# Performance work log

Measured on AMD Instinct MI355X. Metric: run time of the kernel, lower is better.

The kernel has to match this reference:

```python
import jax, jax.numpy as jnp
import numpy as np

# --- module constants (from init_kwargs) ---
BETA = 0.95
UTE = 1.0001
DELAY = 7
CHOSEN_W1 = 0.5
THRESHOLD = 1.0      # snntorch Leaky default threshold
ALPHA = 2.0          # snntorch ATan surrogate default alpha
T, B = 4096, 4096
SPIKE_PROB = 0.02    # sparse binary spike trains


@jax.custom_vjp
def spike_fn(x):
    # Heaviside forward; ATan surrogate gradient in backward (snntorch default)
    return (x > 0).astype(x.dtype)

def _spike_fwd(x):
    return spike_fn(x), x

def _spike_bwd(x, g):
    return (g * (ALPHA / 2.0) / (1.0 + (jnp.pi / 2.0 * ALPHA * x) ** 2),)

spike_fn.defvjp(_spike_fwd, _spike_bwd)


def setup_inputs() -> dict:
    key = jax.random.key(0)
    k1, _ = jax.random.split(key)
    spike_seq = (jax.random.uniform(k1, (T, B, 2)) < SPIKE_PROB).astype(jnp.float32)
    # calculate_weights(delay): w1 = chosen_w1; w2 = ute - beta**delay * w1
    w1 = CHOSEN_W1
    w2 = UTE - BETA ** DELAY * w1
    W = jnp.array([[w1, w2]], dtype=jnp.float32)  # fc.weight, shape [1, 2]
    return {"spike_seq": spike_seq, "W": W}


def reference(spike_seq, W):
    # spike_seq: [T, B, 2], W: [1, 2] -> spk_rec: [T, B, 1]
    # Precompute all linear currents in one GEMM (same math as per-step fc)
    cur_seq = jnp.einsum('tbi,oi->tbo', spike_seq, W)  # [T, B, 1]

    def step(mem, cur):
        # snntorch Leaky (reset_mechanism='subtract'):
        #   reset computed from PREVIOUS mem (detached heaviside)
        reset = (mem > THRESHOLD).astype(mem.dtype)
        mem_new = BETA * mem + cur - reset * THRESHOLD
        spk = spike_fn(mem_new - THRESHOLD)
        return mem_new, spk

    mem0 = jnp.zeros((spike_seq.shape[1], 1), dtype=spike_seq.dtype)
    _, spk_rec = jax.lax.scan(step, mem0, cur_seq)
    return spk_rec
```

## Files before the change

kernel.cpp:

```cpp
#include <hip/hip_runtime.h>
#include <stdint.h>


#define T_STEPS 4096
#define B_NEUR  4096
#define NCHUNK  32
#define CH_W    8
#define WARM_W  48
#define KG      (T_STEPS / 16)
#define NWORDS  (T_STEPS / 32)

typedef float f4v __attribute__((ext_vector_type(4)));

__global__ __launch_bounds__(256) void fmfm_compress(
    const f4v*  __restrict__ sp4,
    uint32_t*   __restrict__ codes)
{
    const int tid = blockIdx.x * 256 + threadIdx.x;
    const int b2  = tid & (B_NEUR / 2 - 1);
    const int kg  = tid >> 11;
    const f4v* p = sp4 + (size_t)kg * 16 * (B_NEUR / 2) + b2;
    uint32_t we = 0, wo = 0;
    #pragma unroll
    for (int i = 0; i < 16; ++i) {
        f4v s = __builtin_nontemporal_load(p + (size_t)i * (B_NEUR / 2));
        uint32_t ce = (s.x != 0.0f ? 1u : 0u) | (s.y != 0.0f ? 2u : 0u);
        uint32_t co = (s.z != 0.0f ? 1u : 0u) | (s.w != 0.0f ? 2u : 0u);
        we |= ce << (2 * i);
        wo |= co << (2 * i);
    }
    *reinterpret_cast<uint2*>(codes + (size_t)kg * B_NEUR + 2 * b2) =
        make_uint2(we, wo);
}

__global__ __launch_bounds__(256, 2) void fmfm_scanA(
    const uint32_t* __restrict__ codes,
    const float*    __restrict__ W,
    uint32_t*       __restrict__ bits_out,
    uint4*          __restrict__ spec)
{
    __shared__ float2 lut2[16];

    const float w1  = W[0];
    const float w2  = W[1];
    const float w12 = __fadd_rn(w1, w2);

    if (threadIdx.x < 16) {
        uint32_t e = threadIdx.x;
        uint32_t c0 = e & 3u, c1 = (e >> 2) & 3u;
        float2 v;
        v.x = (c0 & 1u) ? ((c0 & 2u) ? w12 : w1) : ((c0 & 2u) ? w2 : 0.0f);
        v.y = (c1 & 1u) ? ((c1 & 2u) ? w12 : w1) : ((c1 & 2u) ? w2 : 0.0f);
        lut2[e] = v;
    }
    __syncthreads();

    const int tid = blockIdx.x * 256 + threadIdx.x;
    const int b   = tid & (B_NEUR - 1);
    const int c   = tid >> 12;
    const int body_w0 = c * CH_W;
    const int w_start = (body_w0 >= WARM_W) ? body_w0 - WARM_W : 0;
    const int w_end   = body_w0 + CH_W;
    const uint32_t* cp = codes + b;

#define CLD(IDX) cp[(size_t)((IDX) < w_end ? (IDX) : (w_end - 1)) * B_NEUR]
#define DECODE2(WORD, D)                                                  \
    {                                                                     \
        _Pragma("unroll")                                                 \
        for (int _j = 0; _j < 8; ++_j)                                    \
            D[_j] = lut2[((WORD) >> (4 * _j)) & 0xFu];                    \
    }
#define STEPN(CUR)                                                        \
    {                                                                     \
        float _m = __fsub_rn(__fadd_rn(__fmul_rn(0.95f, mem), (CUR)),     \
                             rst);                                        \
        rst = (_m > 1.0f) ? 1.0f : 0.0f;                                  \
        mem = _m;                                                         \
    }
#define STEPB(CUR, POS)                                                   \
    {                                                                     \
        float _m = __fsub_rn(__fadd_rn(__fmul_rn(0.95f, mem), (CUR)),     \
                             rst);                                        \
        uint32_t _sb = (_m > 1.0f) ? 1u : 0u;                             \
        bits |= _sb << (POS);                                             \
        rst = _sb ? 1.0f : 0.0f;                                          \
        mem = _m;                                                         \
    }
#define CHAIN16N(D)                                                       \
    {                                                                     \
        _Pragma("unroll")                                                 \
        for (int _j = 0; _j < 8; ++_j) { STEPN(D[_j].x) STEPN(D[_j].y) }  \
    }
#define CHAIN16B(D, HALF)                                                 \
    {                                                                     \
        _Pragma("unroll")                                                 \
        for (int _j = 0; _j < 8; ++_j) {                                  \
            STEPB(D[_j].x, ((HALF) << 4) + 2 * _j)                        \
            STEPB(D[_j].y, ((HALF) << 4) + 2 * _j + 1)                    \
        }                                                                 \
    }
#define PF8(G)                                                            \
    t0 = CLD((G) + 8);  t1 = CLD((G) + 9);  t2 = CLD((G) + 10);           \
    t3 = CLD((G) + 11); t4 = CLD((G) + 12); t5 = CLD((G) + 13);           \
    t6 = CLD((G) + 14); t7 = CLD((G) + 15);
#define ROT8()                                                            \
    c0 = t0; c1 = t1; c2 = t2; c3 = t3;                                   \
    c4 = t4; c5 = t5; c6 = t6; c7 = t7;
#define STB(IDX) bits_out[(size_t)(IDX) * B_NEUR + b] = bits;

    uint32_t c0 = CLD(w_start);     uint32_t c1 = CLD(w_start + 1);
    uint32_t c2 = CLD(w_start + 2); uint32_t c3 = CLD(w_start + 3);
    uint32_t c4 = CLD(w_start + 4); uint32_t c5 = CLD(w_start + 5);
    uint32_t c6 = CLD(w_start + 6); uint32_t c7 = CLD(w_start + 7);
    uint32_t t0, t1, t2, t3, t4, t5, t6, t7;

    float2 dA[8], dB[8];
    DECODE2(c0, dA)

    float mem = 0.0f, rst = 0.0f;

    for (int g = w_start; g < body_w0; g += 8) {
        PF8(g)
        DECODE2(c1, dB) CHAIN16N(dA)
        DECODE2(c2, dA) CHAIN16N(dB)
        DECODE2(c3, dB) CHAIN16N(dA)
        DECODE2(c4, dA) CHAIN16N(dB)
        DECODE2(c5, dB) CHAIN16N(dA)
        DECODE2(c6, dA) CHAIN16N(dB)
        DECODE2(c7, dB) CHAIN16N(dA)
        DECODE2(t0, dA) CHAIN16N(dB)
        ROT8()
    }

    const float sm = mem;
    const float sr = rst;

    for (int g = body_w0; g < w_end; g += 8) {
        PF8(g)
        uint32_t bits = 0;
        DECODE2(c1, dB) CHAIN16B(dA, 0)
        DECODE2(c2, dA) CHAIN16B(dB, 1) STB((g + 1) >> 1) bits = 0;
        DECODE2(c3, dB) CHAIN16B(dA, 0)
        DECODE2(c4, dA) CHAIN16B(dB, 1) STB((g + 3) >> 1) bits = 0;
        DECODE2(c5, dB) CHAIN16B(dA, 0)
        DECODE2(c6, dA) CHAIN16B(dB, 1) STB((g + 5) >> 1) bits = 0;
        DECODE2(c7, dB) CHAIN16B(dA, 0)
        DECODE2(t0, dA) CHAIN16B(dB, 1) STB((g + 7) >> 1)
        ROT8()
    }

    uint4 sv;
    sv.x = __float_as_uint(sm);
    sv.y = (sr != 0.0f) ? 1u : 0u;
    sv.z = __float_as_uint(mem);
    sv.w = (rst != 0.0f) ? 1u : 0u;
    spec[(size_t)c * B_NEUR + b] = sv;

#undef CLD
#undef DECODE2
#undef STEPN
#undef STEPB
#undef CHAIN16N
#undef CHAIN16B
#undef PF8
#undef ROT8
#undef STB
}

__global__ __launch_bounds__(64) void fmfm_scanB(
    const uint32_t* __restrict__ codes,
    const float*    __restrict__ W,
    uint32_t*       __restrict__ bits_out,
    const uint4*    __restrict__ spec)
{
    const int b = blockIdx.x * 64 + threadIdx.x;
    const float w1  = W[0];
    const float w2  = W[1];
    const float w12 = __fadd_rn(w1, w2);

    float mem = 0.0f, rst = 0.0f;
    uint4 sn = spec[b];
    for (int c = 0; c < NCHUNK; ++c) {
        uint4 s = sn;
        if (c + 1 < NCHUNK) sn = spec[(size_t)(c + 1) * B_NEUR + b];
        bool ok = (s.x == __float_as_uint(mem)) &&
                  ((s.y != 0u) == (rst != 0.0f));
        if (ok) {
            mem = __uint_as_float(s.z);
            rst = s.w ? 1.0f : 0.0f;
        } else {
            uint32_t bits = 0;
            for (int wi = 0; wi < CH_W; ++wi) {
                uint32_t w = codes[(size_t)(c * CH_W + wi) * B_NEUR + b];
                #pragma unroll
                for (int j = 0; j < 16; ++j) {
                    uint32_t cc = (w >> (2 * j)) & 3u;
                    float cur = (cc & 1u) ? ((cc & 2u) ? w12 : w1)
                                          : ((cc & 2u) ? w2 : 0.0f);
                    float m = __fsub_rn(__fadd_rn(__fmul_rn(0.95f, mem), cur),
                                        rst);
                    uint32_t sb = (m > 1.0f) ? 1u : 0u;
                    bits |= sb << (((wi & 1) << 4) + j);
                    rst = sb ? 1.0f : 0.0f;
                    mem = m;
                }
                if (wi & 1) {
                    bits_out[(size_t)((c * CH_W + wi) >> 1) * B_NEUR + b] = bits;
                    bits = 0;
                }
            }
        }
    }
}

__global__ __launch_bounds__(256) void fmfm_expand(
    const uint32_t* __restrict__ bits,
    float*          __restrict__ out)
{
    const int tid = blockIdx.x * 256 + threadIdx.x;
    const int b4  = tid & 1023;
    const int w   = (tid >> 10) & 127;
    const int q   = tid >> 17;
    const uint4 bw = *reinterpret_cast<const uint4*>(
        bits + (size_t)w * B_NEUR + (size_t)b4 * 4);
    float* qp = out + ((size_t)w * 32 + q * 8) * B_NEUR + (size_t)b4 * 4;
    #pragma unroll
    for (int r = 0; r < 8; ++r) {
        const int tp = q * 8 + r;
        f4v v;
        v.x = ((bw.x >> tp) & 1u) ? 1.0f : 0.0f;
        v.y = ((bw.y >> tp) & 1u) ? 1.0f : 0.0f;
        v.z = ((bw.z >> tp) & 1u) ? 1.0f : 0.0f;
        v.w = ((bw.w >> tp) & 1u) ? 1.0f : 0.0f;
        *reinterpret_cast<f4v*>(qp + (size_t)r * B_NEUR) = v;
    }
}

__global__ __launch_bounds__(64) void fmfm_scan_fused(
    const float2* __restrict__ sp, const float* __restrict__ W,
    float* __restrict__ out)
{
    const int b = blockIdx.x * 64 + threadIdx.x;
    const float w1 = W[0];
    const float w2 = W[1];
    const float2* p = sp + b;
    float* q = out + b;
    float mem = 0.0f, rst = 0.0f;
    #pragma unroll 8
    for (int t = 0; t < T_STEPS; ++t) {
        float2 s = p[(size_t)t * B_NEUR];
        float cur = __fadd_rn(__fmul_rn(s.x, w1), __fmul_rn(s.y, w2));
        float m = __fsub_rn(__fadd_rn(__fmul_rn(0.95f, mem), cur), rst);
        float spk = (m > 1.0f) ? 1.0f : 0.0f;
        q[(size_t)t * B_NEUR] = spk;
        mem = m;
        rst = spk;
    }
}

extern "C" void kernel_launch(void* const* d_in, const int* in_sizes, int n_in,
                              void* d_out, int out_size, void* d_ws, size_t ws_size,
                              hipStream_t stream) {
    const f4v*   sp4 = (const f4v*)d_in[0];
    const float* W   = (const float*)d_in[1];
    float*       out = (float*)d_out;

    const size_t codes_bytes = (size_t)KG * B_NEUR * 4;
    const size_t bits_bytes  = (size_t)NWORDS * B_NEUR * 4;
    const size_t spec_bytes  = (size_t)NCHUNK * B_NEUR * 16;
    if (ws_size < codes_bytes + bits_bytes + spec_bytes) {
        fmfm_scan_fused<<<dim3(B_NEUR / 64), dim3(64), 0, stream>>>(
            (const float2*)d_in[0], W, out);
        return;
    }
    uint32_t* codes = (uint32_t*)d_ws;
    uint32_t* bits  = (uint32_t*)((char*)d_ws + codes_bytes);
    uint4*    spec  = (uint4*)((char*)d_ws + codes_bytes + bits_bytes);

    fmfm_compress<<<dim3(KG * (B_NEUR / 2) / 256), dim3(256), 0, stream>>>(sp4, codes);
    fmfm_scanA<<<dim3(NCHUNK * B_NEUR / 256), dim3(256), 0, stream>>>(codes, W, bits, spec);
    fmfm_scanB<<<dim3(B_NEUR / 64), dim3(64), 0, stream>>>(codes, W, bits, spec);
    fmfm_expand<<<dim3(NWORDS * (B_NEUR / 4) * 4 / 256), dim3(256), 0, stream>>>(bits, out);
}
```

Measured before the change: 66.86 us.

## Interleave two independent chunk scans per thread in speculative scan kernel

Each thread of the chunked speculative scan now processes two chunks (c and c+16) at once, interleaving their recurrence steps to expose instruction-level parallelism across two dependent chains. The grid halves to 256 blocks of 256 threads, occupancy hint drops to one block per SIMD group, and the warm-up window handling is restructured with zero-padding for negative indices. This trades thread-level parallelism for ILP and more registers, aiming to hide the serial FP latency of the membrane chain.

```diff
diff --git a/kernel.cpp b/kernel.cpp
--- a/kernel.cpp
+++ b/kernel.cpp
@@ -33,7 +33,7 @@
         make_uint2(we, wo);
 }
 
-__global__ __launch_bounds__(256, 2) void fmfm_scanA(
+__global__ __launch_bounds__(256, 1) void fmfm_scanA2(
     const uint32_t* __restrict__ codes,
     const float*    __restrict__ W,
     uint32_t*       __restrict__ bits_out,
@@ -47,124 +47,148 @@
 
     if (threadIdx.x < 16) {
         uint32_t e = threadIdx.x;
-        uint32_t c0 = e & 3u, c1 = (e >> 2) & 3u;
+        uint32_t q0 = e & 3u, q1 = (e >> 2) & 3u;
         float2 v;
-        v.x = (c0 & 1u) ? ((c0 & 2u) ? w12 : w1) : ((c0 & 2u) ? w2 : 0.0f);
-        v.y = (c1 & 1u) ? ((c1 & 2u) ? w12 : w1) : ((c1 & 2u) ? w2 : 0.0f);
+        v.x = (q0 & 1u) ? ((q0 & 2u) ? w12 : w1) : ((q0 & 2u) ? w2 : 0.0f);
+        v.y = (q1 & 1u) ? ((q1 & 2u) ? w12 : w1) : ((q1 & 2u) ? w2 : 0.0f);
         lut2[e] = v;
     }
     __syncthreads();
 
     const int tid = blockIdx.x * 256 + threadIdx.x;
     const int b   = tid & (B_NEUR - 1);
-    const int c   = tid >> 12;
-    const int body_w0 = c * CH_W;
-    const int w_start = (body_w0 >= WARM_W) ? body_w0 - WARM_W : 0;
-    const int w_end   = body_w0 + CH_W;
-    const uint32_t* cp = codes + b;
-
-#define CLD(IDX) cp[(size_t)((IDX) < w_end ? (IDX) : (w_end - 1)) * B_NEUR]
+    const int cpair = tid >> 12;
+    const int cA  = cpair;
+    const int cB  = cpair + 16;
+    const int wA0 = cA * CH_W - WARM_W;
+    const int wB0 = cB * CH_W - WARM_W;
+    const uint32_t* cptr = codes + b;
+
+#define FA(V) (((wA0 + (V)) < 0) ? 0u                                     \
+                : cptr[(size_t)(wA0 + (V)) * B_NEUR])
+#define FB(V) cptr[(size_t)(wB0 + (V)) * B_NEUR]
 #define DECODE2(WORD, D)                                                  \
     {                                                                     \
         _Pragma("unroll")                                                 \
         for (int _j = 0; _j < 8; ++_j)                                    \
             D[_j] = lut2[((WORD) >> (4 * _j)) & 0xFu];                    \
     }
-#define STEPN(CUR)                                                        \
-    {                                                                     \
-        float _m = __fsub_rn(__fadd_rn(__fmul_rn(0.95f, mem), (CUR)),     \
-                             rst);                                        \
-        rst = (_m > 1.0f) ? 1.0f : 0.0f;                                  \
-        mem = _m;                                                         \
-    }
-#define STEPB(CUR, POS)                                                   \
-    {                                                                     \
-        float _m = __fsub_rn(__fadd_rn(__fmul_rn(0.95f, mem), (CUR)),     \
-                             rst);                                        \
+#define STEPN_A(CUR)                                                      \
+    {                                                                     \
+        float _m = __fsub_rn(__fadd_rn(__fmul_rn(0.95f, memA), (CUR)),    \
+                             rstA);                                       \
+        rstA = (_m > 1.0f) ? 1.0f : 0.0f;                                 \
+        memA = _m;                                                        \
+    }
+#define STEPN_B(CUR)                                                      \
+    {                                                                     \
+        float _m = __fsub_rn(__fadd_rn(__fmul_rn(0.95f, memB), (CUR)),    \
+                             rstB);                                       \
+        rstB = (_m > 1.0f) ? 1.0f : 0.0f;                                 \
+        memB = _m;                                                        \
+    }
+#define STEPB_A(CUR, POS)                                                 \
+    {                                                                     \
+        float _m = __fsub_rn(__fadd_rn(__fmul_rn(0.95f, memA), (CUR)),    \
+                             rstA);                                       \
         uint32_t _sb = (_m > 1.0f) ? 1u : 0u;                             \
-        bits |= _sb << (POS);                                             \
-        rst = _sb ? 1.0f : 0.0f;                                          \
-        mem = _m;                                                         \
-    }
-#define CHAIN16N(D)                                                       \
-    {                                                                     \
-        _Pragma("unroll")                                                 \
-        for (int _j = 0; _j < 8; ++_j) { STEPN(D[_j].x) STEPN(D[_j].y) }  \
-    }
-#define CHAIN16B(D, HALF)                                                 \
+        bitsA |= _sb << (POS);                                            \
+        rstA = _sb ? 1.0f : 0.0f;                                         \
+        memA = _m;                                                        \
+    }
+#define STEPB_B(CUR, POS)                                                 \
+    {                                                                     \
+        float _m = __fsub_rn(__fadd_rn(__fmul_rn(0.95f, memB), (CUR)),    \
+                             rstB);                                       \
+        uint32_t _sb = (_m > 1.0f) ? 1u : 0u;                             \
+        bitsB |= _sb << (POS);                                            \
+        rstB = _sb ? 1.0f : 0.0f;                                         \
+        memB = _m;                                                        \
+    }
+#define CH2N(DA, DB)                                                      \
     {                                                                     \
         _Pragma("unroll")                                                 \
         for (int _j = 0; _j < 8; ++_j) {                                  \
-            STEPB(D[_j].x, ((HALF) << 4) + 2 * _j)                        \
-            STEPB(D[_j].y, ((HALF) << 4) + 2 * _j + 1)                    \
+            STEPN_A(DA[_j].x) STEPN_B(DB[_j].x)                           \
+            STEPN_A(DA[_j].y) STEPN_B(DB[_j].y)                           \
         }                                                                 \
     }
-#define PF8(G)                                                            \
-    t0 = CLD((G) + 8);  t1 = CLD((G) + 9);  t2 = CLD((G) + 10);           \
-    t3 = CLD((G) + 11); t4 = CLD((G) + 12); t5 = CLD((G) + 13);           \
-    t6 = CLD((G) + 14); t7 = CLD((G) + 15);
-#define ROT8()                                                            \
-    c0 = t0; c1 = t1; c2 = t2; c3 = t3;                                   \
-    c4 = t4; c5 = t5; c6 = t6; c7 = t7;
-#define STB(IDX) bits_out[(size_t)(IDX) * B_NEUR + b] = bits;
-
-    uint32_t c0 = CLD(w_start);     uint32_t c1 = CLD(w_start + 1);
-    uint32_t c2 = CLD(w_start + 2); uint32_t c3 = CLD(w_start + 3);
-    uint32_t c4 = CLD(w_start + 4); uint32_t c5 = CLD(w_start + 5);
-    uint32_t c6 = CLD(w_start + 6); uint32_t c7 = CLD(w_start + 7);
-    uint32_t t0, t1, t2, t3, t4, t5, t6, t7;
-
-    float2 dA[8], dB[8];
-    DECODE2(c0, dA)
-
-    float mem = 0.0f, rst = 0.0f;
-
-    for (int g = w_start; g < body_w0; g += 8) {
-        PF8(g)
-        DECODE2(c1, dB) CHAIN16N(dA)
-        DECODE2(c2, dA) CHAIN16N(dB)
-        DECODE2(c3, dB) CHAIN16N(dA)
-        DECODE2(c4, dA) CHAIN16N(dB)
-        DECODE2(c5, dB) CHAIN16N(dA)
-        DECODE2(c6, dA) CHAIN16N(dB)
-        DECODE2(c7, dB) CHAIN16N(dA)
-        DECODE2(t0, dA) CHAIN16N(dB)
-        ROT8()
-    }
-
-    const float sm = mem;
-    const float sr = rst;
-
-    for (int g = body_w0; g < w_end; g += 8) {
-        PF8(g)
-        uint32_t bits = 0;
-        DECODE2(c1, dB) CHAIN16B(dA, 0)
-        DECODE2(c2, dA) CHAIN16B(dB, 1) STB((g + 1) >> 1) bits = 0;
-        DECODE2(c3, dB) CHAIN16B(dA, 0)
-        DECODE2(c4, dA) CHAIN16B(dB, 1) STB((g + 3) >> 1) bits = 0;
-        DECODE2(c5, dB) CHAIN16B(dA, 0)
-        DECODE2(c6, dA) CHAIN16B(dB, 1) STB((g + 5) >> 1) bits = 0;
-        DECODE2(c7, dB) CHAIN16B(dA, 0)
-        DECODE2(t0, dA) CHAIN16B(dB, 1) STB((g + 7) >> 1)
-        ROT8()
-    }
-
-    uint4 sv;
-    sv.x = __float_as_uint(sm);
-    sv.y = (sr != 0.0f) ? 1u : 0u;
-    sv.z = __float_as_uint(mem);
-    sv.w = (rst != 0.0f) ? 1u : 0u;
-    spec[(size_t)c * B_NEUR + b] = sv;
-
-#undef CLD
+#define CH2B(DA, DB, HALF)                                                \
+    {                                                                     \
+        _Pragma("unroll")                                                 \
+        for (int _j = 0; _j < 8; ++_j) {                                  \
+            STEPB_A(DA[_j].x, ((HALF) << 4) + 2 * _j)                     \
+            STEPB_B(DB[_j].x, ((HALF) << 4) + 2 * _j)                     \
+            STEPB_A(DA[_j].y, ((HALF) << 4) + 2 * _j + 1)                 \
+            STEPB_B(DB[_j].y, ((HALF) << 4) + 2 * _j + 1)                 \
+        }                                                                 \
+    }
+
+    uint32_t a1 = FA(1), a2 = FA(2), a3 = FA(3), a4 = FA(4),
+             a5 = FA(5), a6 = FA(6), a7 = FA(7);
+    uint32_t b1 = FB(1), b2 = FB(2), b3 = FB(3), b4 = FB(4),
+             b5 = FB(5), b6 = FB(6), b7 = FB(7);
+    float2 dA0[8], dA1[8], dB0[8], dB1[8];
+    {
+        uint32_t wa0v = FA(0), wb0v = FB(0);
+        DECODE2(wa0v, dA0)
+        DECODE2(wb0v, dB0)
+    }
+
+    float memA = 0.0f, rstA = 0.0f, memB = 0.0f, rstB = 0.0f;
+
+    for (int g = 0; g < WARM_W; g += 8) {
+        uint32_t tA0 = FA(g + 8),  tA1 = FA(g + 9),  tA2 = FA(g + 10),
+                 tA3 = FA(g + 11), tA4 = FA(g + 12), tA5 = FA(g + 13),
+                 tA6 = FA(g + 14), tA7 = FA(g + 15);
+        uint32_t tB0 = FB(g + 8),  tB1 = FB(g + 9),  tB2 = FB(g + 10),
+                 tB3 = FB(g + 11), tB4 = FB(g + 12), tB5 = FB(g + 13),
+                 tB6 = FB(g + 14), tB7 = FB(g + 15);
+        DECODE2(a1, dA1) DECODE2(b1, dB1) CH2N(dA0, dB0)
+        DECODE2(a2, dA0) DECODE2(b2, dB0) CH2N(dA1, dB1)
+        DECODE2(a3, dA1) DECODE2(b3, dB1) CH2N(dA0, dB0)
+        DECODE2(a4, dA0) DECODE2(b4, dB0) CH2N(dA1, dB1)
+        DECODE2(a5, dA1) DECODE2(b5, dB1) CH2N(dA0, dB0)
+        DECODE2(a6, dA0) DECODE2(b6, dB0) CH2N(dA1, dB1)
+        DECODE2(a7, dA1) DECODE2(b7, dB1) CH2N(dA0, dB0)
+        DECODE2(tA0, dA0) DECODE2(tB0, dB0) CH2N(dA1, dB1)
+        a1 = tA1; a2 = tA2; a3 = tA3; a4 = tA4; a5 = tA5; a6 = tA6; a7 = tA7;
+        b1 = tB1; b2 = tB2; b3 = tB3; b4 = tB4; b5 = tB5; b6 = tB6; b7 = tB7;
+    }
+
+    const float smA = memA, srA = rstA, smB = memB, srB = rstB;
+
+    uint32_t bitsA = 0, bitsB = 0;
+#define STBA(I) bits_out[(size_t)(cA * 4 + (I)) * B_NEUR + b] = bitsA; bitsA = 0;
+#define STBB(I) bits_out[(size_t)(cB * 4 + (I)) * B_NEUR + b] = bitsB; bitsB = 0;
+    DECODE2(a1, dA1) DECODE2(b1, dB1) CH2B(dA0, dB0, 0)
+    DECODE2(a2, dA0) DECODE2(b2, dB0) CH2B(dA1, dB1, 1) STBA(0) STBB(0)
+    DECODE2(a3, dA1) DECODE2(b3, dB1) CH2B(dA0, dB0, 0)
+    DECODE2(a4, dA0) DECODE2(b4, dB0) CH2B(dA1, dB1, 1) STBA(1) STBB(1)
+    DECODE2(a5, dA1) DECODE2(b5, dB1) CH2B(dA0, dB0, 0)
+    DECODE2(a6, dA0) DECODE2(b6, dB0) CH2B(dA1, dB1, 1) STBA(2) STBB(2)
+    DECODE2(a7, dA1) DECODE2(b7, dB1) CH2B(dA0, dB0, 0)
+                                      CH2B(dA1, dB1, 1) STBA(3) STBB(3)
+
+    uint4 svA, svB;
+    svA.x = __float_as_uint(smA); svA.y = (srA != 0.0f) ? 1u : 0u;
+    svA.z = __float_as_uint(memA); svA.w = (rstA != 0.0f) ? 1u : 0u;
+    svB.x = __float_as_uint(smB); svB.y = (srB != 0.0f) ? 1u : 0u;
+    svB.z = __float_as_uint(memB); svB.w = (rstB != 0.0f) ? 1u : 0u;
+    spec[(size_t)cA * B_NEUR + b] = svA;
+    spec[(size_t)cB * B_NEUR + b] = svB;
+
+#undef FA
+#undef FB
 #undef DECODE2
-#undef STEPN
-#undef STEPB
-#undef CHAIN16N
-#undef CHAIN16B
-#undef PF8
-#undef ROT8
-#undef STB
+#undef STEPN_A
+#undef STEPN_B
+#undef STEPB_A
+#undef STEPB_B
+#undef CH2N
+#undef CH2B
+#undef STBA
+#undef STBB
 }
 
 __global__ __launch_bounds__(64) void fmfm_scanB(
@@ -278,7 +302,7 @@
     uint4*    spec  = (uint4*)((char*)d_ws + codes_bytes + bits_bytes);
 
     fmfm_compress<<<dim3(KG * (B_NEUR / 2) / 256), dim3(256), 0, stream>>>(sp4, codes);
-    fmfm_scanA<<<dim3(NCHUNK * B_NEUR / 256), dim3(256), 0, stream>>>(codes, W, bits, spec);
+    fmfm_scanA2<<<dim3(256), dim3(256), 0, stream>>>(codes, W, bits, spec);
     fmfm_scanB<<<dim3(B_NEUR / 64), dim3(64), 0, stream>>>(codes, W, bits, spec);
     fmfm_expand<<<dim3(NWORDS * (B_NEUR / 4) * 4 / 256), dim3(256), 0, stream>>>(bits, out);
 }
```

New measurement: 78.37 us. 1.17x slower.
